# Kernel tuning notes

Measured on AMD Instinct MI355X. Metric: run time of the kernel, lower is better.

Reference implementation:

```python
import jax, jax.numpy as jnp
import numpy as np

N_NODES = 50000
N_EDGES = 800000
IN_FEATS = 128
OUT_FEATS = 128
HEADS = 2
EW_DIMS = 2
NEG_SLOPE = 0.2


def setup_inputs() -> dict:
    key = jax.random.key(0)
    ks = jax.random.split(key, 8)
    feat = jax.random.normal(ks[0], (N_NODES, IN_FEATS), dtype=jnp.float32)
    e_w = jax.random.uniform(ks[1], (N_EDGES, EW_DIMS), dtype=jnp.float32)
    src = jax.random.randint(ks[2], (N_EDGES,), 0, N_NODES)
    dst = jax.random.randint(ks[3], (N_EDGES,), 0, N_NODES)
    # Learned params: per-head fc weight, attn vectors (xavier-ish scale)
    s = 1.0 / np.sqrt(IN_FEATS)
    W = jax.random.normal(ks[4], (HEADS, OUT_FEATS, IN_FEATS), dtype=jnp.float32) * s
    attn_l = jax.random.normal(ks[5], (HEADS, OUT_FEATS), dtype=jnp.float32) * s
    attn_r = jax.random.normal(ks[6], (HEADS, OUT_FEATS), dtype=jnp.float32) * s
    attn_ew = jax.random.normal(ks[7], (HEADS, EW_DIMS), dtype=jnp.float32)
    return {"feat": feat, "e_w": e_w, "src": src, "dst": dst,
            "W": W, "attn_l": attn_l, "attn_r": attn_r, "attn_ew": attn_ew}


def reference(feat, e_w, src, dst, W, attn_l, attn_r, attn_ew):
    N = feat.shape[0]
    # per-head projection: [N, H, O]
    ft = jnp.einsum('nf,hof->nho', feat, W)
    el = jnp.einsum('nho,ho->nh', ft, attn_l)           # [N, H]
    er = jnp.einsum('nho,ho->nh', ft, attn_r)           # [N, H]
    ew = jnp.einsum('ed,hd->eh', e_w, attn_ew)          # [E, H]
    # u_add_v + edge-weight attention + leaky_relu
    e = jax.nn.leaky_relu(el[src] + er[dst] + ew, NEG_SLOPE)  # [E, H]
    # edge_softmax grouped by destination node (numerically stable)
    emax = jax.ops.segment_max(e, dst, num_segments=N)
    emax = jnp.where(jnp.isfinite(emax), emax, 0.0)
    ee = jnp.exp(e - emax[dst])
    denom = jax.ops.segment_sum(ee, dst, num_segments=N)
    a = ee / jnp.where(denom[dst] > 0, denom[dst], 1.0)       # [E, H]
    # u_mul_e / sum aggregation: [N, H, O]
    m = ft[src] * a[:, :, None]
    rst = jax.ops.segment_sum(m, dst, num_segments=N)
    # residual (Identity since in_feats == out_feats) + elu, then cat heads
    rst = jax.nn.elu(rst + feat[:, None, :])
    return rst.reshape(N, -1)
```

## Files before the change

### kernel.cpp

```cpp
#include <hip/hip_runtime.h>
#include <math.h>

#define NNODES 50000
#define NEDGES 800000
#define INF 128
#define OUTF 128
#define HEADS 2
#define NEG_SLOPE 0.2f

#define CAP 32
#define OVFCAP 32768

__device__ __forceinline__ unsigned short f2bf(float f) {
    unsigned u = __float_as_uint(f);
    unsigned r = (u + 0x7FFFu + ((u >> 16) & 1u)) >> 16;
    return (unsigned short)r;
}
__device__ __forceinline__ float bf2f(unsigned short b) {
    return __uint_as_float((unsigned)b << 16);
}
__device__ __forceinline__ unsigned cvt_pk_bf16(float lo, float hi) {
    unsigned r;
    asm("v_cvt_pk_bf16_f32 %0, %1, %2" : "=v"(r) : "v"(lo), "v"(hi));
    return r;
}

typedef __attribute__((ext_vector_type(8))) short frag_ab;
typedef __attribute__((ext_vector_type(4))) float frag_cd;
typedef __attribute__((ext_vector_type(8))) unsigned short ushort8v;

#define APITCH 136

__global__ void init_kernel(const float* __restrict__ W,
                            const float* __restrict__ attn_l,
                            const float* __restrict__ attn_r,
                            unsigned short* __restrict__ Wb,
                            float* __restrict__ wfold) {
    const int b = blockIdx.x, t = threadIdx.x;
    if (b == 0) {
        int h = t >> 7, f = t & 127;
        float sl = 0.f, sr = 0.f;
#pragma unroll 16
        for (int o = 0; o < 128; ++o) {
            float wv = W[(size_t)(h * 128 + o) * 128 + f];
            sl = fmaf(attn_l[h * 128 + o], wv, sl);
            sr = fmaf(attn_r[h * 128 + o], wv, sr);
        }
        wfold[h * 128 + f] = sl;
        wfold[(2 + h) * 128 + f] = sr;
        return;
    }
    int base = (b - 1) * 4096 + t * 16;
#pragma unroll
    for (int q = 0; q < 4; ++q) {
        float4 g = *(const float4*)(W + base + q * 4);
        ushort4 v; v.x = f2bf(g.x); v.y = f2bf(g.y); v.z = f2bf(g.z); v.w = f2bf(g.w);
        *(ushort4*)(Wb + base + q * 4) = v;
    }
}

__global__ __launch_bounds__(256) void prep_kernel(const float* __restrict__ feat,
                                                   const float* __restrict__ wfold,
                                                   float* __restrict__ el,
                                                   float* __restrict__ er,
                                                   int* __restrict__ cursor,
                                                   int* __restrict__ ovfcnt, int N) {
    const int t = threadIdx.x;
    const int gtid = blockIdx.x * 256 + t;
    if (gtid < N) cursor[gtid] = 0;
    if (gtid == 0) *ovfcnt = 0;
    const int lid = t & 31;
    const int n = blockIdx.x * 8 + (t >> 5);
    if (n >= N) return;
    float4 f4 = *(const float4*)(feat + (size_t)n * INF + lid * 4);
    float pd[4];
#pragma unroll
    for (int vq = 0; vq < 4; ++vq) {
        float4 wv = *(const float4*)(wfold + vq * 128 + lid * 4);
        pd[vq] = f4.x * wv.x + f4.y * wv.y + f4.z * wv.z + f4.w * wv.w;
    }
#pragma unroll
    for (int m = 1; m < 32; m <<= 1)
#pragma unroll
        for (int vq = 0; vq < 4; ++vq) pd[vq] += __shfl_xor(pd[vq], m, 64);
    if (lid == 0) {
        *(float2*)(el + (size_t)n * 2) = make_float2(pd[0], pd[1]);
        *(float2*)(er + (size_t)n * 2) = make_float2(pd[2], pd[3]);
    }
}

__global__ __launch_bounds__(512) void fused_gemm_edge(
        const float* __restrict__ feat, const unsigned short* __restrict__ Wb,
        unsigned short* __restrict__ ftb,
        const float* __restrict__ el, const float* __restrict__ er,
        const float* __restrict__ e_w, const int* __restrict__ src,
        const int* __restrict__ dst, const float* __restrict__ attn_ew,
        int* __restrict__ cursor, int* __restrict__ ovfcnt,
        uint2* __restrict__ edata, float4* __restrict__ ovf,
        int N, int E) {
    __shared__ unsigned short Bs[256 * APITCH];
    const int t = threadIdx.x;
    const int lane = t & 63;
    const int m16 = lane & 15, quad = lane >> 4;
    const int n0 = blockIdx.x * 128;

    frag_ab af[2][4];
    bool vr0 = false, vr1 = false;
    int r0n = 0, r1n = 0;
    if (t < 256) {
        const int w = t >> 6;
        r0n = n0 + w * 16 + m16;
        r1n = r0n + 64;
        vr0 = r0n < N; vr1 = r1n < N;
#pragma unroll
        for (int kc = 0; kc < 4; ++kc) {
            const int cc = kc * 32 + quad * 8;
            float4 ga0 = make_float4(0.f, 0.f, 0.f, 0.f), ga1 = ga0;
            float4 gb0 = ga0, gb1 = ga0;
            if (vr0) {
                ga0 = *(const float4*)(feat + (size_t)r0n * INF + cc);
                ga1 = *(const float4*)(feat + (size_t)r0n * INF + cc + 4);
            }
            if (vr1) {
                gb0 = *(const float4*)(feat + (size_t)r1n * INF + cc);
                gb1 = *(const float4*)(feat + (size_t)r1n * INF + cc + 4);
            }
            union { int4 i; frag_ab f; } ua, ub;
            ua.i.x = (int)cvt_pk_bf16(ga0.x, ga0.y); ua.i.y = (int)cvt_pk_bf16(ga0.z, ga0.w);
            ua.i.z = (int)cvt_pk_bf16(ga1.x, ga1.y); ua.i.w = (int)cvt_pk_bf16(ga1.z, ga1.w);
            ub.i.x = (int)cvt_pk_bf16(gb0.x, gb0.y); ub.i.y = (int)cvt_pk_bf16(gb0.z, gb0.w);
            ub.i.z = (int)cvt_pk_bf16(gb1.x, gb1.y); ub.i.w = (int)cvt_pk_bf16(gb1.z, gb1.w);
            af[0][kc] = ua.f; af[1][kc] = ub.f;
        }
    }

#pragma unroll
    for (int i = 0; i < 8; ++i) {
        int q = t + i * 512;
        int row = q >> 4, c = q & 15;
        ushort8v v = *(const ushort8v*)(Wb + row * 128 + c * 8);
        *(ushort8v*)(&Bs[row * APITCH + c * 8]) = v;
    }
    __syncthreads();

    if (t < 256) {
#pragma unroll 1
        for (int jt = 0; jt < 4; ++jt) {
            frag_cd acc[2][4];
#pragma unroll
            for (int rg = 0; rg < 2; ++rg)
#pragma unroll
                for (int nt = 0; nt < 4; ++nt) acc[rg][nt] = frag_cd{0.f, 0.f, 0.f, 0.f};
#pragma unroll
            for (int kc = 0; kc < 4; ++kc)
#pragma unroll
                for (int nt = 0; nt < 4; ++nt) {
                    frag_ab bf = *(const frag_ab*)(&Bs[(jt * 64 + nt * 16 + m16) * APITCH
                                                       + kc * 32 + quad * 8]);
                    acc[0][nt] = __builtin_amdgcn_mfma_f32_16x16x32_bf16(bf, af[0][kc],
                                                                         acc[0][nt], 0, 0, 0);
                    acc[1][nt] = __builtin_amdgcn_mfma_f32_16x16x32_bf16(bf, af[1][kc],
                                                                         acc[1][nt], 0, 0, 0);
                }
#pragma unroll
            for (int rg = 0; rg < 2; ++rg) {
                const int rr = rg ? r1n : r0n;
                if (rg ? vr1 : vr0) {
#pragma unroll
                    for (int nt = 0; nt < 4; ++nt) {
                        uint2 p;
                        p.x = cvt_pk_bf16(acc[rg][nt][0], acc[rg][nt][1]);
                        p.y = cvt_pk_bf16(acc[rg][nt][2], acc[rg][nt][3]);
                        *(uint2*)(ftb + (size_t)rr * 256 + jt * 64 + nt * 16 + quad * 4) = p;
                    }
                }
            }
        }
    } else {
        const float aew0 = attn_ew[0], aew1 = attn_ew[1];
        const float aew2 = attn_ew[2], aew3 = attn_ew[3];
        const int stride = gridDim.x * 256;
        for (int e = blockIdx.x * 256 + (t - 256); e < E; e += stride) {
            int s = src[e], d = dst[e];
            float2 ew2 = *(const float2*)(e_w + (size_t)e * 2);
            float2 elv = *(const float2*)(el + (size_t)s * 2);
            float2 erv = *(const float2*)(er + (size_t)d * 2);
            float v0 = elv.x + erv.x + ew2.x * aew0 + ew2.y * aew1;
            float v1 = elv.y + erv.y + ew2.x * aew2 + ew2.y * aew3;
            v0 = v0 >= 0.f ? v0 : NEG_SLOPE * v0;
            v1 = v1 >= 0.f ? v1 : NEG_SLOPE * v1;
            float ee0 = __expf(v0);
            float ee1 = __expf(v1);
            int pos = atomicAdd(cursor + d, 1);
            if (pos < CAP) {
                unsigned pk = ((unsigned)f2bf(ee1) << 16) | (unsigned)f2bf(ee0);
                edata[(size_t)d * CAP + pos] = make_uint2((unsigned)s, pk);
            } else {
                int o = atomicAdd(ovfcnt, 1);
                if (o < OVFCAP)
                    ovf[o] = make_float4(__int_as_float(d), __int_as_float(s), ee0, ee1);
            }
        }
    }
}

__global__ __launch_bounds__(256) void aggregate(const unsigned short* __restrict__ ftb,
                                                 const float* __restrict__ feat,
                                                 const uint2* __restrict__ edata,
                                                 const int* __restrict__ cursor,
                                                 const int* __restrict__ ovfcnt,
                                                 const float4* __restrict__ ovf,
                                                 float* __restrict__ out, int N) {
    const int t = threadIdx.x;
    const int w = t >> 6, l = t & 63;
    const int n = blockIdx.x * 4 + w;
    if (n >= N) return;
    const int c0 = 4 * l;
    const int h = l >> 5;
    const int cnt = cursor[n];
    const int cmain = cnt < CAP ? cnt : CAP;
    const uint2* eb = edata + (size_t)n * CAP;

    float4 acc = make_float4(0.f, 0.f, 0.f, 0.f);
    float dn = 0.f;
#pragma unroll 4
    for (int i = 0; i < cmain; ++i) {
        uint2 rec = eb[i];
        int s = (int)rec.x;
        float a = bf2f((unsigned short)(h ? (rec.y >> 16) : (rec.y & 0xFFFFu)));
        dn += a;
        ushort4 v = *(const ushort4*)(ftb + (size_t)s * 256 + c0);
        acc.x += a * bf2f(v.x);
        acc.y += a * bf2f(v.y);
        acc.z += a * bf2f(v.z);
        acc.w += a * bf2f(v.w);
    }
    if (cnt > CAP) {
        int no = *ovfcnt; if (no > OVFCAP) no = OVFCAP;
        for (int i = 0; i < no; ++i) {
            float4 ov = ovf[i];
            if (__float_as_int(ov.x) == n) {
                int s = __float_as_int(ov.y);
                float a = h ? ov.w : ov.z;
                dn += a;
                ushort4 v = *(const ushort4*)(ftb + (size_t)s * 256 + c0);
                acc.x += a * bf2f(v.x);
                acc.y += a * bf2f(v.y);
                acc.z += a * bf2f(v.z);
                acc.w += a * bf2f(v.w);
            }
        }
    }
    float inv = dn > 0.f ? 1.0f / dn : 0.f;
    float4 f4 = *(const float4*)(feat + (size_t)n * INF + (c0 & 127));
    float4 r;
    r.x = acc.x * inv + f4.x;
    r.y = acc.y * inv + f4.y;
    r.z = acc.z * inv + f4.z;
    r.w = acc.w * inv + f4.w;
    r.x = r.x > 0.f ? r.x : expm1f(r.x);
    r.y = r.y > 0.f ? r.y : expm1f(r.y);
    r.z = r.z > 0.f ? r.z : expm1f(r.z);
    r.w = r.w > 0.f ? r.w : expm1f(r.w);
    *(float4*)(out + (size_t)n * 256 + c0) = r;
}

extern "C" void kernel_launch(void* const* d_in, const int* in_sizes, int n_in,
                              void* d_out, int out_size, void* d_ws, size_t ws_size,
                              hipStream_t stream) {
    const float* feat    = (const float*)d_in[0];
    const float* e_w     = (const float*)d_in[1];
    const int*   src     = (const int*)d_in[2];
    const int*   dst     = (const int*)d_in[3];
    const float* W       = (const float*)d_in[4];
    const float* attn_l  = (const float*)d_in[5];
    const float* attn_r  = (const float*)d_in[6];
    const float* attn_ew = (const float*)d_in[7];
    float* out = (float*)d_out;

    const int N = in_sizes[0] / INF;
    const int E = in_sizes[2];

    unsigned short* ftb = (unsigned short*)d_ws;
    uint2*  edata  = (uint2*)(ftb + (size_t)N * 256);
    float*  el     = (float*)(edata + (size_t)N * CAP);
    float*  er     = el + (size_t)N * 2;
    float*  wfold  = er + (size_t)N * 2;
    unsigned short* Wb = (unsigned short*)(wfold + 512);
    float4* ovf    = (float4*)(Wb + 32768);
    int*    cursor = (int*)(ovf + OVFCAP);
    int*    ovfcnt = cursor + N;

    init_kernel<<<9, 256, 0, stream>>>(W, attn_l, attn_r, Wb, wfold);

    prep_kernel<<<(N + 7) / 8, 256, 0, stream>>>(feat, wfold, el, er, cursor, ovfcnt, N);

    fused_gemm_edge<<<(N + 127) / 128, 512, 0, stream>>>(feat, Wb, ftb, el, er, e_w,
                                                         src, dst, attn_ew,
                                                         cursor, ovfcnt, edata, ovf, N, E);

    aggregate<<<(N + 3) / 4, 256, 0, stream>>>(ftb, feat, edata, cursor, ovfcnt, ovf, out, N);
}
```

Measured before the change: 214.6 us.

## Bin edges per XCD with workgroup-scope atomics and a shared spill bin

Replaces the single per-destination cursor and 32-slot edge bucket with per-XCD cursors and 4-slot bins, selected by reading the hardware XCC id. Edges that overflow go to a shared 16-slot bin per node, then to the global overflow list. The per-XCD cursors use relaxed workgroup-scope atomics, so the atomic traffic from edge scattering should stay local to each XCD's L2 instead of contending across dies. The cost is that aggregate must read eight cursors and walk nine small bins per node, which adds loop overhead and scattered record reads. Correctness depends on the XCC-id register and the assumption that all workgroups on one XCD share that L2.

```diff
diff --git a/kernel.cpp b/kernel.cpp
--- a/kernel.cpp
+++ b/kernel.cpp
@@ -8,7 +8,9 @@
 #define HEADS 2
 #define NEG_SLOPE 0.2f
 
-#define CAP 32
+#define NXCD 8
+#define PCAP 4
+#define SCAPS 16
 #define OVFCAP 32768
 
 __device__ __forceinline__ unsigned short f2bf(float f) {
@@ -63,12 +65,10 @@
                                                    const float* __restrict__ wfold,
                                                    float* __restrict__ el,
                                                    float* __restrict__ er,
-                                                   int* __restrict__ cursor,
-                                                   int* __restrict__ ovfcnt, int N) {
+                                                   int* __restrict__ curx, int N) {
     const int t = threadIdx.x;
     const int gtid = blockIdx.x * 256 + t;
-    if (gtid < N) cursor[gtid] = 0;
-    if (gtid == 0) *ovfcnt = 0;
+    if (gtid < (NXCD + 1) * N + 1) curx[gtid] = 0;
     const int lid = t & 31;
     const int n = blockIdx.x * 8 + (t >> 5);
     if (n >= N) return;
@@ -95,8 +95,8 @@
         const float* __restrict__ el, const float* __restrict__ er,
         const float* __restrict__ e_w, const int* __restrict__ src,
         const int* __restrict__ dst, const float* __restrict__ attn_ew,
-        int* __restrict__ cursor, int* __restrict__ ovfcnt,
-        uint2* __restrict__ edata, float4* __restrict__ ovf,
+        int* __restrict__ curx, int* __restrict__ scur, int* __restrict__ ovfcnt,
+        uint2* __restrict__ pbin, uint2* __restrict__ sbin, float4* __restrict__ ovf,
         int N, int E) {
     __shared__ unsigned short Bs[256 * APITCH];
     const int t = threadIdx.x;
@@ -177,6 +177,10 @@
             }
         }
     } else {
+        unsigned xcc;
+        asm volatile("s_getreg_b32 %0, hwreg(HW_REG_XCC_ID)" : "=s"(xcc));
+        xcc &= (NXCD - 1);
+        const size_t cxb = (size_t)xcc * N;
         const float aew0 = attn_ew[0], aew1 = attn_ew[1];
         const float aew2 = attn_ew[2], aew3 = attn_ew[3];
         const int stride = gridDim.x * 256;
@@ -191,14 +195,21 @@
             v1 = v1 >= 0.f ? v1 : NEG_SLOPE * v1;
             float ee0 = __expf(v0);
             float ee1 = __expf(v1);
-            int pos = atomicAdd(cursor + d, 1);
-            if (pos < CAP) {
-                unsigned pk = ((unsigned)f2bf(ee1) << 16) | (unsigned)f2bf(ee0);
-                edata[(size_t)d * CAP + pos] = make_uint2((unsigned)s, pk);
+            unsigned pk = ((unsigned)f2bf(ee1) << 16) | (unsigned)f2bf(ee0);
+            uint2 rec = make_uint2((unsigned)s, pk);
+            int pos = __hip_atomic_fetch_add(curx + cxb + d, 1,
+                                             __ATOMIC_RELAXED, __HIP_MEMORY_SCOPE_WORKGROUP);
+            if (pos < PCAP) {
+                pbin[(cxb + d) * PCAP + pos] = rec;
             } else {
-                int o = atomicAdd(ovfcnt, 1);
-                if (o < OVFCAP)
-                    ovf[o] = make_float4(__int_as_float(d), __int_as_float(s), ee0, ee1);
+                int ps = atomicAdd(scur + d, 1);
+                if (ps < SCAPS) {
+                    sbin[(size_t)d * SCAPS + ps] = rec;
+                } else {
+                    int o = atomicAdd(ovfcnt, 1);
+                    if (o < OVFCAP)
+                        ovf[o] = make_float4(__int_as_float(d), __int_as_float(s), ee0, ee1);
+                }
             }
         }
     }
@@ -206,8 +217,10 @@
 
 __global__ __launch_bounds__(256) void aggregate(const unsigned short* __restrict__ ftb,
                                                  const float* __restrict__ feat,
-                                                 const uint2* __restrict__ edata,
-                                                 const int* __restrict__ cursor,
+                                                 const uint2* __restrict__ pbin,
+                                                 const uint2* __restrict__ sbin,
+                                                 const int* __restrict__ curx,
+                                                 const int* __restrict__ scur,
                                                  const int* __restrict__ ovfcnt,
                                                  const float4* __restrict__ ovf,
                                                  float* __restrict__ out, int N) {
@@ -217,25 +230,36 @@
     if (n >= N) return;
     const int c0 = 4 * l;
     const int h = l >> 5;
-    const int cnt = cursor[n];
-    const int cmain = cnt < CAP ? cnt : CAP;
-    const uint2* eb = edata + (size_t)n * CAP;
+    int cx[NXCD];
+#pragma unroll
+    for (int x = 0; x < NXCD; ++x) cx[x] = curx[(size_t)x * N + n];
+    const int scr = scur[n];
 
     float4 acc = make_float4(0.f, 0.f, 0.f, 0.f);
     float dn = 0.f;
-#pragma unroll 4
-    for (int i = 0; i < cmain; ++i) {
-        uint2 rec = eb[i];
-        int s = (int)rec.x;
-        float a = bf2f((unsigned short)(h ? (rec.y >> 16) : (rec.y & 0xFFFFu)));
-        dn += a;
-        ushort4 v = *(const ushort4*)(ftb + (size_t)s * 256 + c0);
-        acc.x += a * bf2f(v.x);
-        acc.y += a * bf2f(v.y);
-        acc.z += a * bf2f(v.z);
-        acc.w += a * bf2f(v.w);
-    }
-    if (cnt > CAP) {
+#define BODY(RECEXPR)                                                          \
+    {   uint2 rec = (RECEXPR);                                                 \
+        int s = (int)rec.x;                                                    \
+        float a = bf2f((unsigned short)(h ? (rec.y >> 16) : (rec.y & 0xFFFFu)));\
+        dn += a;                                                               \
+        ushort4 v = *(const ushort4*)(ftb + (size_t)s * 256 + c0);             \
+        acc.x += a * bf2f(v.x);                                                \
+        acc.y += a * bf2f(v.y);                                                \
+        acc.z += a * bf2f(v.z);                                                \
+        acc.w += a * bf2f(v.w);                                                \
+    }
+#pragma unroll
+    for (int x = 0; x < NXCD; ++x) {
+        const int cc = cx[x] < PCAP ? cx[x] : PCAP;
+        const uint2* pb = pbin + ((size_t)x * N + n) * PCAP;
+        for (int j = 0; j < cc; ++j) BODY(pb[j]);
+    }
+    {
+        const int sc = scr < SCAPS ? scr : SCAPS;
+        const uint2* sb = sbin + (size_t)n * SCAPS;
+        for (int j = 0; j < sc; ++j) BODY(sb[j]);
+    }
+    if (scr > SCAPS) {
         int no = *ovfcnt; if (no > OVFCAP) no = OVFCAP;
         for (int i = 0; i < no; ++i) {
             float4 ov = ovf[i];
@@ -251,6 +275,7 @@
             }
         }
     }
+#undef BODY
     float inv = dn > 0.f ? 1.0f / dn : 0.f;
     float4 f4 = *(const float4*)(feat + (size_t)n * INF + (c0 & 127));
     float4 r;
@@ -282,22 +307,26 @@
     const int E = in_sizes[2];
 
     unsigned short* ftb = (unsigned short*)d_ws;
-    uint2*  edata  = (uint2*)(ftb + (size_t)N * 256);
-    float*  el     = (float*)(edata + (size_t)N * CAP);
+    uint2*  pbin   = (uint2*)(ftb + (size_t)N * 256);
+    uint2*  sbin   = pbin + (size_t)NXCD * N * PCAP;
+    float*  el     = (float*)(sbin + (size_t)N * SCAPS);
     float*  er     = el + (size_t)N * 2;
     float*  wfold  = er + (size_t)N * 2;
     unsigned short* Wb = (unsigned short*)(wfold + 512);
     float4* ovf    = (float4*)(Wb + 32768);
-    int*    cursor = (int*)(ovf + OVFCAP);
-    int*    ovfcnt = cursor + N;
+    int*    curx   = (int*)(ovf + OVFCAP);
+    int*    scur   = curx + (size_t)NXCD * N;
+    int*    ovfcnt = scur + N;
 
     init_kernel<<<9, 256, 0, stream>>>(W, attn_l, attn_r, Wb, wfold);
 
-    prep_kernel<<<(N + 7) / 8, 256, 0, stream>>>(feat, wfold, el, er, cursor, ovfcnt, N);
+    prep_kernel<<<(N + 7) / 8, 256, 0, stream>>>(feat, wfold, el, er, curx, N);
 
     fused_gemm_edge<<<(N + 127) / 128, 512, 0, stream>>>(feat, Wb, ftb, el, er, e_w,
                                                          src, dst, attn_ew,
-                                                         cursor, ovfcnt, edata, ovf, N, E);
-
-    aggregate<<<(N + 3) / 4, 256, 0, stream>>>(ftb, feat, edata, cursor, ovfcnt, ovf, out, N);
-}
+                                                         curx, scur, ovfcnt,
+                                                         pbin, sbin, ovf, N, E);
+
+    aggregate<<<(N + 3) / 4, 256, 0, stream>>>(ftb, feat, pbin, sbin, curx, scur,
+                                               ovfcnt, ovf, out, N);
+}
```

Result: slower. 259.3 us (+20.8%).
